# Kernel optimization log

Measured on AMD Instinct MI355X. Metric: run time of the kernel, lower is better.

## Reference

```python
import jax, jax.numpy as jnp
import numpy as np

B, T, D, H, d = 2, 2048, 1024, 16, 64
INNER = H * d
SCALE = d ** -0.5


def _rope(x, inv_freq):
    # x: [B, H, T, d], interleaved rotary as in the torch module
    t = x.shape[2]
    pos = jnp.arange(t, dtype=jnp.float32)
    freqs = pos[:, None] * inv_freq[None, :]          # [T, d/2]
    cos_f, sin_f = jnp.cos(freqs), jnp.sin(freqs)
    x1, x2 = x[..., 0::2], x[..., 1::2]
    y1 = x1 * cos_f - x2 * sin_f
    y2 = x1 * sin_f + x2 * cos_f
    return jnp.stack([y1, y2], axis=-1).reshape(x.shape)


def setup_inputs() -> dict:
    key = jax.random.key(0)
    ks = jax.random.split(key, 6)
    x = jax.random.normal(ks[0], (B, T, D), jnp.float32)
    W_qkv = jax.random.normal(ks[1], (D, 3 * INNER), jnp.float32) * (D ** -0.5)
    W_out = jax.random.normal(ks[2], (INNER, D), jnp.float32) * (INNER ** -0.5)
    W_dt = jax.random.normal(ks[3], (D, H), jnp.float32) * 0.01
    b_dt = jnp.full((H,), -4.0, jnp.float32)
    W_gsp = jax.random.normal(ks[4], (D, INNER), jnp.float32) * 0.01
    b_gsp = jnp.full((INNER,), -3.0, jnp.float32)
    inv_freq = 1.0 / (10000.0 ** (jnp.arange(0, d, 2, dtype=jnp.float32) / d))
    return {"x": x, "W_qkv": W_qkv, "W_out": W_out, "W_dt": W_dt,
            "b_dt": b_dt, "W_gsp": W_gsp, "b_gsp": b_gsp, "inv_freq": inv_freq}


def reference(x, W_qkv, W_out, W_dt, b_dt, W_gsp, b_gsp, inv_freq):
    qkv = (x @ W_qkv).reshape(B, T, 3, H, d)
    Q = jnp.moveaxis(qkv[:, :, 0], 1, 2)   # [B,H,T,d]
    K = jnp.moveaxis(qkv[:, :, 1], 1, 2)
    V = jnp.moveaxis(qkv[:, :, 2], 1, 2)
    Q = _rope(Q, inv_freq)
    K = _rope(K, inv_freq)

    dt = jax.nn.softplus(x @ W_dt + b_dt)             # [B,T,H]
    gamma = jnp.moveaxis(jnp.exp(-dt), 1, 2)          # [B,H,T]

    p = jax.nn.sigmoid(x @ W_gsp + b_gsp).reshape(B, T, H, d)
    p = jnp.moveaxis(p, 1, 2)                          # [B,H,T,d]
    gamma_eff = gamma[..., None] * (1.0 - p) + p
    gamma_scalar = gamma_eff.mean(axis=-1)            # [B,H,T]
    V = V * (1.0 - p)

    log_gamma = jnp.log(jnp.clip(gamma_scalar, 1e-6, 1.0 - 1e-6))
    lgc = jnp.cumsum(log_gamma, axis=-1)              # [B,H,T]
    log_D = jnp.clip(lgc[..., :, None] - lgc[..., None, :], -20.0, 0.0)
    causal = jnp.tril(jnp.ones((T, T), jnp.float32))
    Dm = jnp.exp(log_D) * causal                      # [B,H,T,T]

    Wscore = jnp.einsum('bhtd,bhsd->bhts', Q * SCALE, K)
    A = Wscore * Dm
    Y = jnp.einsum('bhts,bhsd->bhtd', A, V)
    Y = jnp.moveaxis(Y, 1, 2).reshape(B, T, INNER)
    return Y @ W_out
```

## Files before the change

### kernel.cpp

```cpp
#include <hip/hip_runtime.h>
#include <hip/hip_bf16.h>
#include <math.h>

#define B_     2
#define T_     2048
#define D_     1024
#define H_     16
#define INNER_ 1024
#define NC_    4096
#define SCALE_ 0.125f

typedef unsigned short u16;
typedef short short8 __attribute__((ext_vector_type(8)));
typedef float f32x4 __attribute__((ext_vector_type(4)));
typedef float f32x16 __attribute__((ext_vector_type(16)));
typedef unsigned short u16x4 __attribute__((ext_vector_type(4)));
typedef unsigned int u32x2 __attribute__((ext_vector_type(2)));

__device__ __forceinline__ u16 f2bf(float x) {
  union { float f; unsigned u; } v; v.f = x;
  unsigned r = v.u + 0x7fffu + ((v.u >> 16) & 1u);
  return (u16)(r >> 16);
}
__device__ __forceinline__ float b2f(u16 x) {
  union { unsigned u; float f; } v; v.u = ((unsigned)x) << 16;
  return v.f;
}
__device__ __forceinline__ unsigned cvtpk(float lo, float hi) {
  unsigned r;
  asm("v_cvt_pk_bf16_f32 %0, %1, %2" : "=v"(r) : "v"(lo), "v"(hi));
  return r;
}
__device__ __forceinline__ void gload16(const void* g, void* l) {
  __builtin_amdgcn_global_load_lds(
      (const __attribute__((address_space(1))) void*)g,
      (__attribute__((address_space(3))) void*)l, 16, 0, 0);
}

__global__ __launch_bounds__(256) void prep_kernel(
    const float* __restrict__ x, const float* __restrict__ W_qkv,
    const float* __restrict__ W_gsp, const float* __restrict__ W_out,
    const float* __restrict__ W_dt, const float* __restrict__ inv_freq,
    u16* __restrict__ xb, u16* __restrict__ Wcombt, u16* __restrict__ Woutt,
    u16* __restrict__ Wdtb, float2* __restrict__ tab) {
  const int bid = blockIdx.x, tid = threadIdx.x;
  if (bid < 1280) {
    const float* src; u16* dst; int N, nx, ky;
    if (bid < 768)       { src = W_qkv; dst = Wcombt;                N = 3072; nx = bid % 48;          ky = bid / 48; }
    else if (bid < 1024) { src = W_gsp; dst = Wcombt + 3072 * 1024;  N = 1024; nx = (bid - 768) % 16;  ky = (bid - 768) / 16; }
    else                 { src = W_out; dst = Woutt;                 N = 1024; nx = (bid - 1024) % 16; ky = (bid - 1024) / 16; }
    __shared__ float tile[64][65];
    const int k0 = ky * 64, n0 = nx * 64;
    for (int e = tid; e < 4096; e += 256) {
      int kk = e >> 6, nn = e & 63;
      tile[kk][nn] = src[(size_t)(k0 + kk) * N + n0 + nn];
    }
    __syncthreads();
    for (int e = tid; e < 4096; e += 256) {
      int nn = e >> 6, kk = e & 63;
      dst[(size_t)(n0 + nn) * 1024 + k0 + kk] = f2bf(tile[kk][nn]);
    }
  } else if (bid < 1344) {
    int i = (bid - 1280) * 256 + tid;
    int k = i >> 4, h = i & 15;
    Wdtb[(size_t)h * D_ + k] = f2bf(W_dt[i]);
  } else if (bid < 1600) {
    int i = (bid - 1344) * 256 + tid;
    int t = i >> 5, j = i & 31;
    float s, c;
    sincosf((float)t * inv_freq[j], &s, &c);
    tab[i] = make_float2(c, s);
  } else {
    int base = (bid - 1600) * 1024 + tid;
#pragma unroll
    for (int r = 0; r < 4; ++r) {
      int i = base + r * 256;
      float4 v = *reinterpret_cast<const float4*>(x + (size_t)i * 4);
      u16x4 o; o.x = f2bf(v.x); o.y = f2bf(v.y); o.z = f2bf(v.z); o.w = f2bf(v.w);
      *reinterpret_cast<u16x4*>(xb + (size_t)i * 4) = o;
    }
  }
}

__global__ __launch_bounds__(256, 2) void gemm_big(
    const u16* __restrict__ A, const u16* __restrict__ Bt,
    u16* __restrict__ C) {
  __shared__ u16 As[2][128 * 32] __attribute__((aligned(16)));
  __shared__ u16 Bs[2][256 * 32] __attribute__((aligned(16)));
  const int tid = threadIdx.x;
  const int w = tid >> 6, l = tid & 63;
  const int bid = blockIdx.x;
  const int xcd = bid & 7, idx = bid >> 3;
  const int brow = xcd * 4 + (idx & 3);
  const int bcol = idx >> 2;
  const int m0 = brow * 128, n0 = bcol * 256;
  const int ql = l & 15, g4 = l >> 4;
  const int srow = tid >> 2;
  const int ssl  = (tid & 3) ^ (srow & 3);

  const u16* Ag = A + (size_t)m0 * D_;
  const u16* Bg = Bt + (size_t)n0 * D_;

  auto STAGE = [&](int kt, int bp) {
#pragma unroll
    for (int c = 0; c < 2; ++c)
      gload16(Ag + (size_t)(c * 64 + srow) * D_ + kt * 32 + ssl * 8,
              (char*)As[bp] + c * 4096 + tid * 16);
#pragma unroll
    for (int c = 0; c < 4; ++c)
      gload16(Bg + (size_t)(c * 64 + srow) * D_ + kt * 32 + ssl * 8,
              (char*)Bs[bp] + c * 4096 + tid * 16);
  };

  f32x4 acc[8][4] = {};
  STAGE(0, 0);

  const int NT = D_ / 32;
  for (int kt = 0; kt < NT; ++kt) {
    const int bp = kt & 1;
    __builtin_amdgcn_s_barrier();
    if (kt + 1 < NT) {
      STAGE(kt + 1, bp ^ 1);
      asm volatile("s_waitcnt vmcnt(6)" ::: "memory");
    } else {
      asm volatile("s_waitcnt vmcnt(0)" ::: "memory");
    }
    __builtin_amdgcn_sched_barrier(0);

    const char* Asb = (const char*)As[bp];
    const char* Bsb = (const char*)Bs[bp];
    short8 bf[4], af[4];
#pragma unroll
    for (int nf = 0; nf < 4; ++nf) {
      int row = w * 64 + nf * 16 + ql;
      bf[nf] = *(const short8*)(Bsb + row * 64 + ((g4 ^ (row & 3)) << 4));
    }
#pragma unroll
    for (int mf = 0; mf < 4; ++mf) {
      int row = mf * 16 + ql;
      af[mf] = *(const short8*)(Asb + row * 64 + ((g4 ^ (row & 3)) << 4));
    }
    __builtin_amdgcn_s_setprio(1);
#pragma unroll
    for (int mf = 0; mf < 4; ++mf)
#pragma unroll
      for (int nf = 0; nf < 4; ++nf)
        acc[mf][nf] = __builtin_amdgcn_mfma_f32_16x16x32_bf16(af[mf], bf[nf], acc[mf][nf], 0, 0, 0);
    __builtin_amdgcn_s_setprio(0);
#pragma unroll
    for (int mf = 0; mf < 4; ++mf) {
      int row = 64 + mf * 16 + ql;
      af[mf] = *(const short8*)(Asb + row * 64 + ((g4 ^ (row & 3)) << 4));
    }
    __builtin_amdgcn_s_setprio(1);
#pragma unroll
    for (int mf = 0; mf < 4; ++mf)
#pragma unroll
      for (int nf = 0; nf < 4; ++nf)
        acc[mf + 4][nf] = __builtin_amdgcn_mfma_f32_16x16x32_bf16(af[mf], bf[nf], acc[mf + 4][nf], 0, 0, 0);
    __builtin_amdgcn_s_setprio(0);
  }

#pragma unroll
  for (int mf = 0; mf < 8; ++mf) {
#pragma unroll
    for (int r = 0; r < 4; ++r) {
      size_t row = (size_t)(m0 + mf * 16 + g4 * 4 + r);
      size_t base = row * NC_ + n0 + w * 64 + ql;
#pragma unroll
      for (int nf = 0; nf < 4; ++nf)
        C[base + nf * 16] = f2bf(acc[mf][nf][r]);
    }
  }
}

template <bool BF16OUT>
__global__ __launch_bounds__(256) void gemm_bt(
    const u16* __restrict__ A, const u16* __restrict__ Bt,
    void* __restrict__ Cv, int M, int N, int K) {
  __shared__ u16 As[2][128 * 64] __attribute__((aligned(16)));
  __shared__ u16 Bs[2][128 * 64] __attribute__((aligned(16)));
  const int tid = threadIdx.x, w = tid >> 6, l = tid & 63;
  const int rpx = (M >> 7) >> 3;
  const int bid = blockIdx.x;
  const int xcd = bid & 7, idx = bid >> 3;
  const int brow = xcd * rpx + (idx % rpx);
  const int bcol = idx / rpx;
  const int m0 = brow * 128, n0 = bcol * 128;
  const int wr = (w >> 1) * 64, wc = (w & 1) * 64;
  const int srow = l >> 3;
  const int kgrp = ((l & 7) ^ srow) * 8;

  f32x4 acc[4][4] = {};

  auto stage = [&](int kt, int bs) {
#pragma unroll
    for (int i = 0; i < 4; ++i) {
      int c = w * 4 + i;
      int row = c * 8 + srow;
      gload16(A + (size_t)(m0 + row) * K + kt * 64 + kgrp, (char*)As[bs] + c * 1024);
      gload16(Bt + (size_t)(n0 + row) * K + kt * 64 + kgrp, (char*)Bs[bs] + c * 1024);
    }
  };

  stage(0, 0);
  const int NT = K >> 6;
  for (int kt = 0; kt < NT; ++kt) {
    if (kt + 1 < NT) {
      stage(kt + 1, (kt + 1) & 1);
      asm volatile("s_waitcnt vmcnt(8)" ::: "memory");
    } else {
      asm volatile("s_waitcnt vmcnt(0)" ::: "memory");
    }
    __builtin_amdgcn_sched_barrier(0);
    __builtin_amdgcn_s_barrier();
    __builtin_amdgcn_sched_barrier(0);
    const char* Asb = (const char*)As[kt & 1];
    const char* Bsb = (const char*)Bs[kt & 1];
#pragma unroll
    for (int kk = 0; kk < 2; ++kk) {
      short8 af[4], bf[4];
#pragma unroll
      for (int i = 0; i < 4; ++i) {
        int ra = wr + i * 16 + (l & 15);
        int sa = kk * 4 + (l >> 4);
        af[i] = *(const short8*)(Asb + ra * 128 + ((sa ^ (ra & 7)) << 4));
        int rb = wc + i * 16 + (l & 15);
        bf[i] = *(const short8*)(Bsb + rb * 128 + ((sa ^ (rb & 7)) << 4));
      }
#pragma unroll
      for (int i = 0; i < 4; ++i)
#pragma unroll
        for (int j = 0; j < 4; ++j)
          acc[i][j] = __builtin_amdgcn_mfma_f32_16x16x32_bf16(af[i], bf[j], acc[i][j], 0, 0, 0);
    }
    if (kt + 1 < NT) __builtin_amdgcn_s_barrier();
  }
#pragma unroll
  for (int i = 0; i < 4; ++i) {
#pragma unroll
    for (int r = 0; r < 4; ++r) {
      size_t row = (size_t)(m0 + wr + i * 16 + (l >> 4) * 4 + r);
      size_t base = row * N + n0 + wc + (l & 15);
#pragma unroll
      for (int j = 0; j < 4; ++j) {
        if (BF16OUT) ((u16*)Cv)[base + j * 16] = f2bf(acc[i][j][r]);
        else         ((float*)Cv)[base + j * 16] = acc[i][j][r];
      }
    }
  }
}

__global__ __launch_bounds__(256) void pointwise_kernel(
    const u16* __restrict__ C, const u16* __restrict__ xb,
    const u16* __restrict__ Wdtb, const float* __restrict__ b_dt,
    const float* __restrict__ b_gsp, const float2* __restrict__ tab,
    u16* __restrict__ Qb, u16* __restrict__ Kb, u16* __restrict__ Vb,
    float* __restrict__ lg) {
  const int row = blockIdx.x * 4 + (threadIdx.x >> 6);
  const int l = threadIdx.x & 63;
  const int b = row >> 11, t = row & (T_ - 1);
  const int h = l >> 2;
  const int dd0 = (l & 3) * 16;
  const int col = h * 64 + dd0;
  const size_t cb = (size_t)row * NC_;

  float gsum = 0.f;
  {
    const int kc = (l & 3) * 256;
    const short8* xpg = (const short8*)(xb + (size_t)row * D_ + kc);
    const short8* wpg = (const short8*)(Wdtb + h * D_ + kc);
#pragma unroll
    for (int i = 0; i < 32; ++i) {
      short8 xv = xpg[i], wv = wpg[i];
#pragma unroll
      for (int j = 0; j < 8; ++j) gsum += b2f((u16)xv[j]) * b2f((u16)wv[j]);
    }
    gsum += __shfl_xor(gsum, 1);
    gsum += __shfl_xor(gsum, 2);
  }
  const float dtv = gsum + b_dt[h];
  const float sp = (dtv > 20.f) ? dtv : log1pf(__expf(dtv));
  const float gh = __expf(-sp);

  const short8* qp = (const short8*)(C + cb + col);
  const short8* kp = (const short8*)(C + cb + 1024 + col);
  const short8* vp = (const short8*)(C + cb + 2048 + col);
  const short8* pp = (const short8*)(C + cb + 3072 + col);
  short8 q0 = qp[0], q1 = qp[1];
  short8 k0 = kp[0], k1 = kp[1];
  short8 v0 = vp[0], v1 = vp[1];
  short8 pr0 = pp[0], pr1 = pp[1];

  float ge = 0.f;
  short8 vo0, vo1;
#pragma unroll
  for (int i = 0; i < 8; ++i) {
    float pv = b2f((u16)pr0[i]) + b_gsp[col + i];
    float p = 1.f / (1.f + __expf(-pv));
    ge += gh * (1.f - p) + p;
    vo0[i] = (short)f2bf(b2f((u16)v0[i]) * (1.f - p));
    float pv1 = b2f((u16)pr1[i]) + b_gsp[col + 8 + i];
    float p1 = 1.f / (1.f + __expf(-pv1));
    ge += gh * (1.f - p1) + p1;
    vo1[i] = (short)f2bf(b2f((u16)v1[i]) * (1.f - p1));
  }
  const size_t hm = (((size_t)(b * H_ + h)) * T_ + t) * 64 + dd0;
  ((short8*)(Vb + hm))[0] = vo0;
  ((short8*)(Vb + hm))[1] = vo1;

  ge += __shfl_xor(ge, 1);
  ge += __shfl_xor(ge, 2);
  if ((l & 3) == 0) {
    float gs = ge * (1.f / 64.f);
    gs = fminf(fmaxf(gs, 1e-6f), 1.f - 1e-6f);
    lg[((size_t)(b * H_ + h)) * T_ + t] = logf(gs);
  }

  short8 qo0, qo1, ko0, ko1;
  const float2* cs = tab + t * 32 + (dd0 >> 1);
#pragma unroll
  for (int m = 0; m < 4; ++m) {
    float2 c0 = cs[m];
    float qa = b2f((u16)q0[2 * m]), qb = b2f((u16)q0[2 * m + 1]);
    qo0[2 * m]     = (short)f2bf((qa * c0.x - qb * c0.y) * SCALE_);
    qo0[2 * m + 1] = (short)f2bf((qa * c0.y + qb * c0.x) * SCALE_);
    float ka = b2f((u16)k0[2 * m]), kb = b2f((u16)k0[2 * m + 1]);
    ko0[2 * m]     = (short)f2bf(ka * c0.x - kb * c0.y);
    ko0[2 * m + 1] = (short)f2bf(ka * c0.y + kb * c0.x);
    float2 c1 = cs[4 + m];
    float qa1 = b2f((u16)q1[2 * m]), qb1 = b2f((u16)q1[2 * m + 1]);
    qo1[2 * m]     = (short)f2bf((qa1 * c1.x - qb1 * c1.y) * SCALE_);
    qo1[2 * m + 1] = (short)f2bf((qa1 * c1.y + qb1 * c1.x) * SCALE_);
    float ka1 = b2f((u16)k1[2 * m]), kb1 = b2f((u16)k1[2 * m + 1]);
    ko1[2 * m]     = (short)f2bf(ka1 * c1.x - kb1 * c1.y);
    ko1[2 * m + 1] = (short)f2bf(ka1 * c1.y + kb1 * c1.x);
  }
  ((short8*)(Qb + hm))[0] = qo0; ((short8*)(Qb + hm))[1] = qo1;
  ((short8*)(Kb + hm))[0] = ko0; ((short8*)(Kb + hm))[1] = ko1;
}

__global__ __launch_bounds__(256) void scan_kernel(
    const float* __restrict__ lg, float* __restrict__ lgc) {
  const size_t base = (size_t)blockIdx.x * T_;
  const int tid = threadIdx.x;
  __shared__ float sums[256];
  float loc[8];
  float run = 0.f;
#pragma unroll
  for (int i = 0; i < 8; ++i) { run += lg[base + tid * 8 + i]; loc[i] = run; }
  sums[tid] = run;
  __syncthreads();
  if (tid == 0) {
    float r = 0.f;
    for (int i = 0; i < 256; ++i) { float v = sums[i]; sums[i] = r; r += v; }
  }
  __syncthreads();
  const float off = sums[tid];
#pragma unroll
  for (int i = 0; i < 8; ++i) lgc[base + tid * 8 + i] = off + loc[i];
}

__global__ __launch_bounds__(256) void kv_prep_kernel(
    const u16* __restrict__ Vb, const float* __restrict__ lgc,
    u16* __restrict__ Vtg) {
  const int stile = blockIdx.x;
  const int bh = blockIdx.y;
  const int tid = threadIdx.x;
  __shared__ u16 vt[64][72];
  const size_t base = ((size_t)bh * T_ + (size_t)stile * 64) * 64;
  const float* lgp = lgc + (size_t)bh * T_;
  const float lgb = lgp[stile * 64];
#pragma unroll
  for (int i = 0; i < 2; ++i) {
    int c = tid * 2 + i;
    int row = c >> 3, k8 = (c & 7) * 8;
    float beta = __expf(lgb - lgp[stile * 64 + row]);
    short8 vv = *(const short8*)(Vb + base + row * 64 + k8);
#pragma unroll
    for (int j = 0; j < 8; ++j) vt[row][k8 + j] = f2bf(b2f((u16)vv[j]) * beta);
  }
  __syncthreads();
#pragma unroll
  for (int i = 0; i < 2; ++i) {
    int c = tid * 2 + i;
    int dd = c >> 3, t8 = (c & 7) * 8;
    short8 o;
#pragma unroll
    for (int j = 0; j < 8; ++j) o[j] = (short)vt[t8 + j][dd];
    *(short8*)(Vtg + ((size_t)(bh * 32 + stile) * 64 + dd) * 64 + t8) = o;
  }
}

__global__ __launch_bounds__(256) void attn_mfma(
    const u16* __restrict__ Qb, const u16* __restrict__ Kb,
    const u16* __restrict__ Vtg, const float* __restrict__ lgc,
    u16* __restrict__ Y) {
  const int i = blockIdx.x;
  const int xcd = i & 7;
  const int half = i >> 8;
  const int r = (i >> 3) & 31;
  const int q8 = r >> 2;
  const int bh_hi = r & 3;
  const int qb = half ? (15 - q8) : q8;
  const int bh = xcd + (bh_hi << 3);
  const int b = bh >> 4, h = bh & 15;
  const int tid = threadIdx.x, w = tid >> 6, l = tid & 63;
  const int l31 = l & 31, hi = l >> 5;
  __shared__ u16 Ks[3][64 * 64] __attribute__((aligned(16)));
  __shared__ u16 Vs[3][64 * 64] __attribute__((aligned(16)));
  __shared__ u16 Ps[4][2048] __attribute__((aligned(16)));
  const u16* Qg = Qb + (size_t)bh * T_ * 64;
  const u16* Kg = Kb + (size_t)bh * T_ * 64;
  const u16* Vg = Vtg + (size_t)bh * 32 * 4096;
  const float* lgp = lgc + (size_t)bh * T_;
  const int srow = l >> 3, slot8 = l & 7;

  const int q0 = qb * 128 + w * 32;
  const int qg = q0 + l31;
  short8 qf[4];
#pragma unroll
  for (int kk = 0; kk < 4; ++kk)
    qf[kk] = *(const short8*)(Qg + (size_t)qg * 64 + kk * 16 + hi * 8);
  const float lgq = lgp[qg];
  const float lgtop = lgp[qb * 128];

  char* Pw = (char*)Ps[w];
  const int psw = l31 & 7;

  f32x16 yacc0 = {}, yacc1 = {};

  const int st0 = qb * 2 + 1;
  int s_min;
  {
    int lo = 0, hic = st0;
    while (lo < hic) {
      int mid = (lo + hic) >> 1;
      if (lgtop - lgp[mid * 64 + 63] > -20.f) hic = mid; else lo = mid + 1;
    }
    s_min = lo;
  }

  auto STAGE = [&](int s) {
    const int bs = s % 3;
#pragma unroll
    for (int i2 = 0; i2 < 2; ++i2) {
      int c = w * 2 + i2, row = c * 8 + srow;
      int kg = (slot8 ^ (row & 7)) * 8;
      gload16(Kg + (size_t)(s * 64 + row) * 64 + kg, (char*)Ks[bs] + c * 1024);
      gload16(Vg + (size_t)s * 4096 + row * 64 + kg, (char*)Vs[bs] + c * 1024);
    }
  };

  STAGE(st0);
  if (st0 - 1 >= s_min) STAGE(st0 - 1);

  for (int st = st0; st >= s_min; --st) {
    __builtin_amdgcn_s_barrier();
    if (st - 2 >= s_min) {
      STAGE(st - 2);
      asm volatile("s_waitcnt vmcnt(8)" ::: "memory");
    } else if (st - 1 >= s_min) {
      asm volatile("s_waitcnt vmcnt(4)" ::: "memory");
    } else {
      asm volatile("s_waitcnt vmcnt(0)" ::: "memory");
    }
    __builtin_amdgcn_sched_barrier(0);

    const bool allinv = (st * 64 > q0 + 31);
    if (!allinv) {
      const int bs = st % 3;
      const char* Ksb = (const char*)Ks[bs];
      const char* Vsb = (const char*)Vs[bs];
      const float alpha = __expf(lgq - lgp[st * 64]);
      const bool domask = (st * 64 + 63 > q0);
      const int qrel = qg - st * 64;
#pragma unroll
      for (int sblk = 0; sblk < 2; ++sblk) {
        f32x16 c = {};
        __builtin_amdgcn_s_setprio(1);
#pragma unroll
        for (int kk = 0; kk < 4; ++kk) {
          int row = sblk * 32 + l31;
          short8 kf = *(const short8*)(Ksb + row * 128 + (((kk * 2 + hi) ^ (row & 7)) << 4));
          c = __builtin_amdgcn_mfma_f32_32x32x16_bf16(kf, qf[kk], c, 0, 0, 0);
        }
        __builtin_amdgcn_s_setprio(0);
        if (domask) {
#pragma unroll
          for (int bq = 0; bq < 4; ++bq) {
            float p0 = c[bq * 4 + 0] * alpha, p1 = c[bq * 4 + 1] * alpha;
            float p2 = c[bq * 4 + 2] * alpha, p3 = c[bq * 4 + 3] * alpha;
            int s64 = sblk * 32 + bq * 8 + hi * 4;
            if (s64 + 0 > qrel) p0 = 0.f;
            if (s64 + 1 > qrel) p1 = 0.f;
            if (s64 + 2 > qrel) p2 = 0.f;
            if (s64 + 3 > qrel) p3 = 0.f;
            u32x2 pk; pk.x = cvtpk(p0, p1); pk.y = cvtpk(p2, p3);
            int slot = sblk * 4 + bq;
            *(u32x2*)(Pw + l31 * 128 + ((slot ^ psw) << 4) + hi * 8) = pk;
          }
        } else {
#pragma unroll
          for (int bq = 0; bq < 4; ++bq) {
            u32x2 pk;
            pk.x = cvtpk(c[bq * 4 + 0] * alpha, c[bq * 4 + 1] * alpha);
            pk.y = cvtpk(c[bq * 4 + 2] * alpha, c[bq * 4 + 3] * alpha);
            int slot = sblk * 4 + bq;
            *(u32x2*)(Pw + l31 * 128 + ((slot ^ psw) << 4) + hi * 8) = pk;
          }
        }
      }
#pragma unroll
      for (int kk = 0; kk < 4; ++kk) {
        short8 pf = *(const short8*)(Pw + l31 * 128 + (((kk * 2 + hi) ^ psw) << 4));
        short8 vf0 = *(const short8*)(Vsb + l31 * 128 + (((kk * 2 + hi) ^ (l31 & 7)) << 4));
        short8 vf1 = *(const short8*)(Vsb + (32 + l31) * 128 + (((kk * 2 + hi) ^ (l31 & 7)) << 4));
        __builtin_amdgcn_s_setprio(1);
        yacc0 = __builtin_amdgcn_mfma_f32_32x32x16_bf16(pf, vf0, yacc0, 0, 0, 0);
        yacc1 = __builtin_amdgcn_mfma_f32_32x32x16_bf16(pf, vf1, yacc1, 0, 0, 0);
        __builtin_amdgcn_s_setprio(0);
      }
    }
  }

#pragma unroll
  for (int reg = 0; reg < 16; ++reg) {
    int qrow = (reg & 3) + 8 * (reg >> 2) + 4 * hi;
    size_t rowg = (size_t)(b * T_) + qb * 128 + w * 32 + qrow;
    Y[rowg * INNER_ + h * 64 + l31] = f2bf(yacc0[reg]);
    Y[rowg * INNER_ + h * 64 + 32 + l31] = f2bf(yacc1[reg]);
  }
}

extern "C" void kernel_launch(void* const* d_in, const int* in_sizes, int n_in,
                              void* d_out, int out_size, void* d_ws, size_t ws_size,
                              hipStream_t stream) {
  const float* x        = (const float*)d_in[0];
  const float* W_qkv    = (const float*)d_in[1];
  const float* W_out    = (const float*)d_in[2];
  const float* W_dt     = (const float*)d_in[3];
  const float* b_dt     = (const float*)d_in[4];
  const float* W_gsp    = (const float*)d_in[5];
  const float* b_gsp    = (const float*)d_in[6];
  const float* inv_freq = (const float*)d_in[7];
  float* out = (float*)d_out;

  const int M = B_ * T_;
  char* p = (char*)d_ws;
  auto alloc = [&](size_t bytes) {
    char* r = p; p += (bytes + 255) & ~(size_t)255; return r;
  };
  u16*    xb    = (u16*)alloc((size_t)M * D_ * 2);
  u16*    Wcombt= (u16*)alloc((size_t)NC_ * D_ * 2);
  u16*    Woutt = (u16*)alloc((size_t)D_ * INNER_ * 2);
  u16*    Wdtb  = (u16*)alloc((size_t)H_ * D_ * 2);
  u16*    Cqkvp = (u16*)alloc((size_t)M * NC_ * 2);
  u16*    Qb    = (u16*)alloc((size_t)B_ * H_ * T_ * 64 * 2);
  u16*    Kb    = (u16*)alloc((size_t)B_ * H_ * T_ * 64 * 2);
  u16*    Vb    = (u16*)alloc((size_t)B_ * H_ * T_ * 64 * 2);
  float*  lg    = (float*)alloc((size_t)B_ * H_ * T_ * 4);
  float*  lgc   = (float*)alloc((size_t)B_ * H_ * T_ * 4);
  float2* tab   = (float2*)alloc((size_t)T_ * 32 * 8);
  u16*    Vtg   = Cqkvp;
  u16*    Yb    = Cqkvp + (size_t)4 * 1024 * 1024;

  prep_kernel<<<2624, 256, 0, stream>>>(x, W_qkv, W_gsp, W_out, W_dt, inv_freq,
                                        xb, Wcombt, Woutt, Wdtb, tab);
  gemm_big<<<512, 256, 0, stream>>>(xb, Wcombt, Cqkvp);

  pointwise_kernel<<<M / 4, 256, 0, stream>>>(Cqkvp, xb, Wdtb, b_dt, b_gsp,
                                              tab, Qb, Kb, Vb, lg);
  scan_kernel<<<B_ * H_, 256, 0, stream>>>(lg, lgc);
  kv_prep_kernel<<<dim3(T_ / 64, B_ * H_), 256, 0, stream>>>(Vb, lgc, Vtg);

  attn_mfma<<<512, 256, 0, stream>>>(Qb, Kb, Vtg, lgc, Yb);

  gemm_bt<false><<<256, 256, 0, stream>>>(Yb, Woutt, out, M, D_, INNER_);
}
```

Baseline: 148.7 us.

## Keep attention P in registers via permlane32 swap and restructure prefetch barriers

In the attention kernel, the score tile P is repacked into MFMA A-operand fragments with permlane32_swap instead of a round trip through shared memory, which removes the Ps LDS buffer. The PV MFMAs are now issued per 32-column score block. In both GEMM kernels and the attention loop, the wait-for-loads moves before the barrier and the next-tile prefetch is issued after it. This drops the trailing second barrier but waits for all outstanding loads each iteration, which reduces how much global loading overlaps with compute in the GEMMs.

```diff
diff --git a/kernel.cpp b/kernel.cpp
--- a/kernel.cpp
+++ b/kernel.cpp
@@ -118,14 +118,11 @@
   const int NT = D_ / 32;
   for (int kt = 0; kt < NT; ++kt) {
     const int bp = kt & 1;
+    asm volatile("s_waitcnt vmcnt(0)" ::: "memory");
+    __builtin_amdgcn_sched_barrier(0);
     __builtin_amdgcn_s_barrier();
-    if (kt + 1 < NT) {
-      STAGE(kt + 1, bp ^ 1);
-      asm volatile("s_waitcnt vmcnt(6)" ::: "memory");
-    } else {
-      asm volatile("s_waitcnt vmcnt(0)" ::: "memory");
-    }
     __builtin_amdgcn_sched_barrier(0);
+    if (kt + 1 < NT) STAGE(kt + 1, bp ^ 1);
 
     const char* Asb = (const char*)As[bp];
     const char* Bsb = (const char*)Bs[bp];
@@ -206,15 +203,12 @@
   stage(0, 0);
   const int NT = K >> 6;
   for (int kt = 0; kt < NT; ++kt) {
-    if (kt + 1 < NT) {
-      stage(kt + 1, (kt + 1) & 1);
-      asm volatile("s_waitcnt vmcnt(8)" ::: "memory");
-    } else {
-      asm volatile("s_waitcnt vmcnt(0)" ::: "memory");
-    }
+    asm volatile("s_waitcnt vmcnt(0)" ::: "memory");
     __builtin_amdgcn_sched_barrier(0);
     __builtin_amdgcn_s_barrier();
     __builtin_amdgcn_sched_barrier(0);
+    if (kt + 1 < NT) stage(kt + 1, (kt + 1) & 1);
+
     const char* Asb = (const char*)As[kt & 1];
     const char* Bsb = (const char*)Bs[kt & 1];
 #pragma unroll
@@ -234,7 +228,6 @@
         for (int j = 0; j < 4; ++j)
           acc[i][j] = __builtin_amdgcn_mfma_f32_16x16x32_bf16(af[i], bf[j], acc[i][j], 0, 0, 0);
     }
-    if (kt + 1 < NT) __builtin_amdgcn_s_barrier();
   }
 #pragma unroll
   for (int i = 0; i < 4; ++i) {
@@ -409,7 +402,6 @@
   const int l31 = l & 31, hi = l >> 5;
   __shared__ u16 Ks[3][64 * 64] __attribute__((aligned(16)));
   __shared__ u16 Vs[3][64 * 64] __attribute__((aligned(16)));
-  __shared__ u16 Ps[4][2048] __attribute__((aligned(16)));
   const u16* Qg = Qb + (size_t)bh * T_ * 64;
   const u16* Kg = Kb + (size_t)bh * T_ * 64;
   const u16* Vg = Vtg + (size_t)bh * 32 * 4096;
@@ -424,9 +416,6 @@
     qf[kk] = *(const short8*)(Qg + (size_t)qg * 64 + kk * 16 + hi * 8);
   const float lgq = lgp[qg];
   const float lgtop = lgp[qb * 128];
-
-  char* Pw = (char*)Ps[w];
-  const int psw = l31 & 7;
 
   f32x16 yacc0 = {}, yacc1 = {};
 
@@ -456,16 +445,12 @@
   if (st0 - 1 >= s_min) STAGE(st0 - 1);
 
   for (int st = st0; st >= s_min; --st) {
+    if (st - 1 >= s_min) asm volatile("s_waitcnt vmcnt(4)" ::: "memory");
+    else                 asm volatile("s_waitcnt vmcnt(0)" ::: "memory");
+    __builtin_amdgcn_sched_barrier(0);
     __builtin_amdgcn_s_barrier();
-    if (st - 2 >= s_min) {
-      STAGE(st - 2);
-      asm volatile("s_waitcnt vmcnt(8)" ::: "memory");
-    } else if (st - 1 >= s_min) {
-      asm volatile("s_waitcnt vmcnt(4)" ::: "memory");
-    } else {
-      asm volatile("s_waitcnt vmcnt(0)" ::: "memory");
-    }
     __builtin_amdgcn_sched_barrier(0);
+    if (st - 2 >= s_min) STAGE(st - 2);
 
     const bool allinv = (st * 64 > q0 + 31);
     if (!allinv) {
@@ -486,40 +471,38 @@
           c = __builtin_amdgcn_mfma_f32_32x32x16_bf16(kf, qf[kk], c, 0, 0, 0);
         }
         __builtin_amdgcn_s_setprio(0);
-        if (domask) {
-#pragma unroll
-          for (int bq = 0; bq < 4; ++bq) {
-            float p0 = c[bq * 4 + 0] * alpha, p1 = c[bq * 4 + 1] * alpha;
-            float p2 = c[bq * 4 + 2] * alpha, p3 = c[bq * 4 + 3] * alpha;
-            int s64 = sblk * 32 + bq * 8 + hi * 4;
-            if (s64 + 0 > qrel) p0 = 0.f;
-            if (s64 + 1 > qrel) p1 = 0.f;
-            if (s64 + 2 > qrel) p2 = 0.f;
-            if (s64 + 3 > qrel) p3 = 0.f;
-            u32x2 pk; pk.x = cvtpk(p0, p1); pk.y = cvtpk(p2, p3);
-            int slot = sblk * 4 + bq;
-            *(u32x2*)(Pw + l31 * 128 + ((slot ^ psw) << 4) + hi * 8) = pk;
+        float pv[16];
+#pragma unroll
+        for (int ii = 0; ii < 16; ++ii) {
+          float p = c[ii] * alpha;
+          if (domask) {
+            int s64 = sblk * 32 + (ii & 3) + 8 * (ii >> 2) + 4 * hi;
+            if (s64 > qrel) p = 0.f;
           }
-        } else {
-#pragma unroll
-          for (int bq = 0; bq < 4; ++bq) {
-            u32x2 pk;
-            pk.x = cvtpk(c[bq * 4 + 0] * alpha, c[bq * 4 + 1] * alpha);
-            pk.y = cvtpk(c[bq * 4 + 2] * alpha, c[bq * 4 + 3] * alpha);
-            int slot = sblk * 4 + bq;
-            *(u32x2*)(Pw + l31 * 128 + ((slot ^ psw) << 4) + hi * 8) = pk;
-          }
+          pv[ii] = p;
         }
-      }
-#pragma unroll
-      for (int kk = 0; kk < 4; ++kk) {
-        short8 pf = *(const short8*)(Pw + l31 * 128 + (((kk * 2 + hi) ^ psw) << 4));
-        short8 vf0 = *(const short8*)(Vsb + l31 * 128 + (((kk * 2 + hi) ^ (l31 & 7)) << 4));
-        short8 vf1 = *(const short8*)(Vsb + (32 + l31) * 128 + (((kk * 2 + hi) ^ (l31 & 7)) << 4));
-        __builtin_amdgcn_s_setprio(1);
-        yacc0 = __builtin_amdgcn_mfma_f32_32x32x16_bf16(pf, vf0, yacc0, 0, 0, 0);
-        yacc1 = __builtin_amdgcn_mfma_f32_32x32x16_bf16(pf, vf1, yacc1, 0, 0, 0);
-        __builtin_amdgcn_s_setprio(0);
+        unsigned A0 = cvtpk(pv[0], pv[1]),  A1 = cvtpk(pv[2], pv[3]);
+        unsigned B0 = cvtpk(pv[4], pv[5]),  B1 = cvtpk(pv[6], pv[7]);
+        u32x2 ra = __builtin_amdgcn_permlane32_swap(A0, B0, false, false);
+        u32x2 rb = __builtin_amdgcn_permlane32_swap(A1, B1, false, false);
+        unsigned C0 = cvtpk(pv[8], pv[9]),  C1 = cvtpk(pv[10], pv[11]);
+        unsigned D0 = cvtpk(pv[12], pv[13]), D1 = cvtpk(pv[14], pv[15]);
+        u32x2 rc = __builtin_amdgcn_permlane32_swap(C0, D0, false, false);
+        u32x2 rd = __builtin_amdgcn_permlane32_swap(C1, D1, false, false);
+        union { unsigned u[4]; short8 s; } f0, f1;
+        f0.u[0] = ra[0]; f0.u[1] = rb[0]; f0.u[2] = ra[1]; f0.u[3] = rb[1];
+        f1.u[0] = rc[0]; f1.u[1] = rd[0]; f1.u[2] = rc[1]; f1.u[3] = rd[1];
+#pragma unroll
+        for (int fi = 0; fi < 2; ++fi) {
+          const short8 pf = fi ? f1.s : f0.s;
+          const int kkg = sblk * 2 + fi;
+          short8 vf0 = *(const short8*)(Vsb + l31 * 128 + (((kkg * 2 + hi) ^ (l31 & 7)) << 4));
+          short8 vf1 = *(const short8*)(Vsb + (32 + l31) * 128 + (((kkg * 2 + hi) ^ (l31 & 7)) << 4));
+          __builtin_amdgcn_s_setprio(1);
+          yacc0 = __builtin_amdgcn_mfma_f32_32x32x16_bf16(pf, vf0, yacc0, 0, 0, 0);
+          yacc1 = __builtin_amdgcn_mfma_f32_32x32x16_bf16(pf, vf1, yacc1, 0, 0, 0);
+          __builtin_amdgcn_s_setprio(0);
+        }
       }
     }
   }
```

Measured after the change: 150.6 us. Within noise of the previous version (+1.3%).

## Fix async-load/barrier ordering in GEMMs and attention; fuse scan into kv_prep

Applied to the files above, without the earlier changes.

In the two GEMMs and the attention loop, each iteration now waits for all outstanding global-to-LDS loads (or all but the current stage), then hits the barrier, and only then issues the next prefetch. Before, the prefetch was issued before the wait, so it could overwrite a buffer other waves were still reading. The cumulative-log scan kernel is folded into kv_prep: every block recomputes the scan for its head in shared memory, and tile 0 writes lgc out. This removes one launch but repeats the scan work per tile, and the stricter wait ordering reduces the load/compute overlap in the GEMMs.

```diff
diff --git a/kernel.cpp b/kernel.cpp
--- a/kernel.cpp
+++ b/kernel.cpp
@@ -118,14 +118,11 @@
   const int NT = D_ / 32;
   for (int kt = 0; kt < NT; ++kt) {
     const int bp = kt & 1;
+    asm volatile("s_waitcnt vmcnt(0)" ::: "memory");
+    __builtin_amdgcn_sched_barrier(0);
     __builtin_amdgcn_s_barrier();
-    if (kt + 1 < NT) {
-      STAGE(kt + 1, bp ^ 1);
-      asm volatile("s_waitcnt vmcnt(6)" ::: "memory");
-    } else {
-      asm volatile("s_waitcnt vmcnt(0)" ::: "memory");
-    }
     __builtin_amdgcn_sched_barrier(0);
+    if (kt + 1 < NT) STAGE(kt + 1, bp ^ 1);
 
     const char* Asb = (const char*)As[bp];
     const char* Bsb = (const char*)Bs[bp];
@@ -206,15 +203,12 @@
   stage(0, 0);
   const int NT = K >> 6;
   for (int kt = 0; kt < NT; ++kt) {
-    if (kt + 1 < NT) {
-      stage(kt + 1, (kt + 1) & 1);
-      asm volatile("s_waitcnt vmcnt(8)" ::: "memory");
-    } else {
-      asm volatile("s_waitcnt vmcnt(0)" ::: "memory");
-    }
+    asm volatile("s_waitcnt vmcnt(0)" ::: "memory");
     __builtin_amdgcn_sched_barrier(0);
     __builtin_amdgcn_s_barrier();
     __builtin_amdgcn_sched_barrier(0);
+    if (kt + 1 < NT) stage(kt + 1, (kt + 1) & 1);
+
     const char* Asb = (const char*)As[kt & 1];
     const char* Bsb = (const char*)Bs[kt & 1];
 #pragma unroll
@@ -234,7 +228,6 @@
         for (int j = 0; j < 4; ++j)
           acc[i][j] = __builtin_amdgcn_mfma_f32_16x16x32_bf16(af[i], bf[j], acc[i][j], 0, 0, 0);
     }
-    if (kt + 1 < NT) __builtin_amdgcn_s_barrier();
   }
 #pragma unroll
   for (int i = 0; i < 4; ++i) {
@@ -340,42 +333,48 @@
   ((short8*)(Kb + hm))[0] = ko0; ((short8*)(Kb + hm))[1] = ko1;
 }
 
-__global__ __launch_bounds__(256) void scan_kernel(
-    const float* __restrict__ lg, float* __restrict__ lgc) {
-  const size_t base = (size_t)blockIdx.x * T_;
+__global__ __launch_bounds__(256) void kv_prep_kernel(
+    const u16* __restrict__ Vb, const float* __restrict__ lg,
+    float* __restrict__ lgc, u16* __restrict__ Vtg) {
+  const int stile = blockIdx.x;
+  const int bh = blockIdx.y;
   const int tid = threadIdx.x;
+  __shared__ u16 vt[64][72];
   __shared__ float sums[256];
+  __shared__ float lgs[T_];
+  const size_t lbase = (size_t)bh * T_;
+
   float loc[8];
-  float run = 0.f;
-#pragma unroll
-  for (int i = 0; i < 8; ++i) { run += lg[base + tid * 8 + i]; loc[i] = run; }
-  sums[tid] = run;
+  {
+    float run = 0.f;
+#pragma unroll
+    for (int i = 0; i < 8; ++i) { run += lg[lbase + tid * 8 + i]; loc[i] = run; }
+    sums[tid] = run;
+  }
   __syncthreads();
   if (tid == 0) {
     float r = 0.f;
     for (int i = 0; i < 256; ++i) { float v = sums[i]; sums[i] = r; r += v; }
   }
   __syncthreads();
-  const float off = sums[tid];
-#pragma unroll
-  for (int i = 0; i < 8; ++i) lgc[base + tid * 8 + i] = off + loc[i];
-}
-
-__global__ __launch_bounds__(256) void kv_prep_kernel(
-    const u16* __restrict__ Vb, const float* __restrict__ lgc,
-    u16* __restrict__ Vtg) {
-  const int stile = blockIdx.x;
-  const int bh = blockIdx.y;
-  const int tid = threadIdx.x;
-  __shared__ u16 vt[64][72];
-  const size_t base = ((size_t)bh * T_ + (size_t)stile * 64) * 64;
-  const float* lgp = lgc + (size_t)bh * T_;
-  const float lgb = lgp[stile * 64];
+  {
+    const float off = sums[tid];
+#pragma unroll
+    for (int i = 0; i < 8; ++i) lgs[tid * 8 + i] = off + loc[i];
+  }
+  __syncthreads();
+  if (stile == 0) {
+#pragma unroll
+    for (int i = 0; i < 8; ++i) lgc[lbase + tid * 8 + i] = lgs[tid * 8 + i];
+  }
+
+  const size_t base = (lbase + (size_t)stile * 64) * 64;
+  const float lgb = lgs[stile * 64];
 #pragma unroll
   for (int i = 0; i < 2; ++i) {
     int c = tid * 2 + i;
     int row = c >> 3, k8 = (c & 7) * 8;
-    float beta = __expf(lgb - lgp[stile * 64 + row]);
+    float beta = __expf(lgb - lgs[stile * 64 + row]);
     short8 vv = *(const short8*)(Vb + base + row * 64 + k8);
 #pragma unroll
     for (int j = 0; j < 8; ++j) vt[row][k8 + j] = f2bf(b2f((u16)vv[j]) * beta);
@@ -456,16 +455,12 @@
   if (st0 - 1 >= s_min) STAGE(st0 - 1);
 
   for (int st = st0; st >= s_min; --st) {
+    if (st - 1 >= s_min) asm volatile("s_waitcnt vmcnt(4)" ::: "memory");
+    else                 asm volatile("s_waitcnt vmcnt(0)" ::: "memory");
+    __builtin_amdgcn_sched_barrier(0);
     __builtin_amdgcn_s_barrier();
-    if (st - 2 >= s_min) {
-      STAGE(st - 2);
-      asm volatile("s_waitcnt vmcnt(8)" ::: "memory");
-    } else if (st - 1 >= s_min) {
-      asm volatile("s_waitcnt vmcnt(4)" ::: "memory");
-    } else {
-      asm volatile("s_waitcnt vmcnt(0)" ::: "memory");
-    }
     __builtin_amdgcn_sched_barrier(0);
+    if (st - 2 >= s_min) STAGE(st - 2);
 
     const bool allinv = (st * 64 > q0 + 31);
     if (!allinv) {
@@ -571,8 +566,7 @@
 
   pointwise_kernel<<<M / 4, 256, 0, stream>>>(Cqkvp, xb, Wdtb, b_dt, b_gsp,
                                               tab, Qb, Kb, Vb, lg);
-  scan_kernel<<<B_ * H_, 256, 0, stream>>>(lg, lgc);
-  kv_prep_kernel<<<dim3(T_ / 64, B_ * H_), 256, 0, stream>>>(Vb, lgc, Vtg);
+  kv_prep_kernel<<<dim3(T_ / 64, B_ * H_), 256, 0, stream>>>(Vb, lg, lgc, Vtg);
 
   attn_mfma<<<512, 256, 0, stream>>>(Qb, Kb, Vtg, lgc, Yb);
 
```

After: 148.5 us. About the same (-0.2%).
